# Performance work log

Hardware: AMD Instinct MI355X
Metric: run time of the kernel (lower is better)

Reference implementation:

```python
import jax, jax.numpy as jnp
import numpy as np

N_WIDTH = 16
N_ORDER = 3
N_ELEMENTS = 64
N_NODES = N_ELEMENTS * N_ORDER + 1  # 193
N_SAMPLES = 4096
X_MIN = 0.0
X_MAX = 1.0
NDIM_IN = 2


def setup_inputs() -> dict:
    key = jax.random.key(0)
    k1, k2 = jax.random.split(key)
    x = jax.random.uniform(k1, (N_SAMPLES, NDIM_IN), dtype=jnp.float32)  # in [x_min, x_max]
    # torch init is zeros; use small random values so outputs/grads are informative
    weight = 0.1 * jax.random.normal(k2, (N_WIDTH, N_NODES, NDIM_IN), dtype=jnp.float32)
    return {"x": x, "weight": weight}


def _lagrange_all(xr, nodes):
    """phi, dphi, ddphi of the (n_order+1) Lagrange basis at xr (S,W,D).
    Returns three arrays of shape (S,W,P,D), P = n_order+1. Loops are over the
    tiny fixed basis size only; everything is vectorized over (S,W,D)."""
    P = len(nodes)
    phi, dphi, ddphi = [], [], []
    for j in range(P):
        # value
        p = jnp.ones_like(xr)
        for m in range(P):
            if m != j:
                p = p * (xr - nodes[m]) / (nodes[j] - nodes[m])
        phi.append(p)
        # first derivative
        y1 = jnp.zeros_like(xr)
        for i in range(P):
            if i == j:
                continue
            k = jnp.full_like(xr, 1.0 / (nodes[j] - nodes[i]))
            for m in range(P):
                if m != i and m != j:
                    k = k * (xr - nodes[m]) / (nodes[j] - nodes[m])
            y1 = y1 + k
        dphi.append(y1)
        # second derivative
        y2 = jnp.zeros_like(xr)
        for i in range(P):
            if i == j:
                continue
            ks = jnp.zeros_like(xr)
            for m in range(P):
                if m != i and m != j:
                    kp = jnp.full_like(xr, 1.0 / (nodes[j] - nodes[m]))
                    for n in range(P):
                        if n != i and n != j and n != m:
                            kp = kp * (xr - nodes[n]) / (nodes[j] - nodes[n])
                    ks = ks + kp
            y2 = y2 + ks / (nodes[j] - nodes[i])
        ddphi.append(y2)
    return jnp.stack(phi, 2), jnp.stack(dphi, 2), jnp.stack(ddphi, 2)


def _forward(x, weight):
    S, W, D, P = N_SAMPLES, N_WIDTH, NDIM_IN, N_ORDER + 1
    xw = jnp.broadcast_to(x[:, None, :], (S, W, D))  # (S,W,D)
    x_shift = (N_NODES - 1) * (xw - X_MIN) / (X_MAX - X_MIN)
    id_el = jnp.clip(jnp.floor(x_shift / N_ORDER), 0, N_ELEMENTS - 1)
    nodes_l = (id_el * N_ORDER).astype(jnp.int32)  # (S,W,D), left node index
    # nodes_r - nodes_l == n_order
    x_ref = 2.0 * (x_shift - nodes_l) / N_ORDER - 1.0
    delta_x = 0.5 * N_ORDER * (X_MAX - X_MIN) / (N_NODES - 1)

    nodes = [float(v) for v in np.linspace(-1.0, 1.0, P)]
    phi_l, dphi_l, ddphi_l = _lagrange_all(x_ref, nodes)  # (S,W,P,D)
    dphi_l = dphi_l / delta_x
    ddphi_l = ddphi_l / (delta_x * delta_x)

    # Scatter local basis values into global node axis (vectorized replacement
    # of the quadruple Python loop in the original).
    ii = jnp.arange(S)[:, None, None, None]
    kk = jnp.arange(W)[None, :, None, None]
    dd = jnp.arange(D)[None, None, None, :]
    pp = nodes_l[:, :, None, :] + jnp.arange(P)[None, None, :, None]  # (S,W,P,D)
    zeros = jnp.zeros((S, W, N_NODES, D), dtype=x.dtype)
    phi = zeros.at[ii, kk, pp, dd].set(phi_l)
    dphi = zeros.at[ii, kk, pp, dd].set(dphi_l)
    ddphi = zeros.at[ii, kk, pp, dd].set(ddphi_l)

    t_ik = jnp.einsum('kpj,ikpj->ik', weight, phi)
    dt_ik = jnp.einsum('kpj,ikpj->ik', weight, dphi)
    ddt_ik = jnp.einsum('kpj,ikpj->ik', weight, ddphi)
    return t_ik, dt_ik, ddt_ik, phi, dphi, ddphi, delta_x


def reference(x, weight):
    # returns (t_ik, dt_ik, ddt_ik, phi_ikpj, dphi_ikpj, ddphi_ikpj, delta_x)
    return _forward(x, weight)
```

## Files before the change

kernel.cpp:

```cpp
#include <hip/hip_runtime.h>

constexpr int S  = 4096;
constexpr int W  = 16;
constexpr int NN = 193;
constexpr int DD = 2;
constexpr int SW = S * W;
constexpr int PHI_OFF = 3 * SW;
constexpr int PHI_SZ  = SW * NN * DD;
constexpr int DX_OFF  = PHI_OFF + 3 * PHI_SZ;

constexpr int ROW_F  = NN * DD;
constexpr int ROW_F2 = NN;
constexpr int CHUNK_F2 = W * ROW_F2;

__global__ __launch_bounds__(256)
void kan_fused_kernel(const float* __restrict__ x,
                      const float* __restrict__ w,
                      float* __restrict__ out) {
    const int i   = blockIdx.x;
    const int tid = threadIdx.x;

    __shared__ __align__(16) float row[3][ROW_F];
    __shared__ float vals[3][DD][4];
    __shared__ int   nls[DD];

    for (int idx = tid; idx < 3 * ROW_F; idx += 256)
        (&row[0][0])[idx] = 0.0f;

    if (tid < DD) {
        const int d = tid;
        float xv = x[i * DD + d];
        float xs = 192.0f * xv;
        float fe = floorf(xs / 3.0f);
        fe = fminf(fmaxf(fe, 0.0f), 63.0f);
        int nl = (int)(fe * 3.0f);
        nls[d] = nl;
        float xr = 2.0f * (xs - (float)nl) / 3.0f - 1.0f;

        float xp1 = xr + 1.0f;
        float xm1 = xr - 1.0f;
        float x2  = xr * xr;
        float x2m = x2 - (1.0f / 9.0f);
        const float c0 = 0.5625f;
        const float c1 = 1.6875f;

        vals[0][d][0] = -c0 * x2m * xm1;
        vals[0][d][1] =  c1 * xp1 * (xr - (1.0f / 3.0f)) * xm1;
        vals[0][d][2] = -c1 * xp1 * (xr + (1.0f / 3.0f)) * xm1;
        vals[0][d][3] =  c0 * xp1 * x2m;

        const float idx1 = 128.0f;
        vals[1][d][0] = -c0 * (3.0f * x2 - 2.0f * xr - (1.0f / 9.0f)) * idx1;
        vals[1][d][1] =  c1 * (3.0f * x2 - (2.0f / 3.0f) * xr - 1.0f) * idx1;
        vals[1][d][2] = -c1 * (3.0f * x2 + (2.0f / 3.0f) * xr - 1.0f) * idx1;
        vals[1][d][3] =  c0 * (3.0f * x2 + 2.0f * xr - (1.0f / 9.0f)) * idx1;

        const float idx2 = 16384.0f;
        vals[2][d][0] = -c0 * (6.0f * xr - 2.0f) * idx2;
        vals[2][d][1] =  c1 * (6.0f * xr - (2.0f / 3.0f)) * idx2;
        vals[2][d][2] = -c1 * (6.0f * xr + (2.0f / 3.0f)) * idx2;
        vals[2][d][3] =  c0 * (6.0f * xr + 2.0f) * idx2;
    }

    __syncthreads();

    if (tid < 24) {
        int a = tid >> 3;
        int r = tid & 7;
        int d = r >> 2;
        int p = r & 3;
        row[a][(nls[d] + p) * DD + d] = vals[a][d][p];
    }

    if (tid < 48) {
        int k = tid / 3;
        int a = tid % 3;
        float s = 0.0f;
#pragma unroll
        for (int d = 0; d < DD; ++d) {
            int base = k * (NN * DD) + nls[d] * DD + d;
#pragma unroll
            for (int p = 0; p < 4; ++p)
                s += w[base + p * DD] * vals[a][d][p];
        }
        out[a * SW + i * W + k] = s;
    }

    if (i == 0 && tid == 0)
        out[DX_OFF] = 0.0078125f;

    __syncthreads();

#pragma unroll
    for (int a = 0; a < 3; ++a) {
        float2* dst = (float2*)(out + PHI_OFF + a * PHI_SZ) + (size_t)i * CHUNK_F2;
        const float2* src = (const float2*)(&row[a][0]);
        for (int idx = tid; idx < CHUNK_F2; idx += 256) {
            int j = idx % ROW_F2;
            dst[idx] = src[j];
        }
    }
}

extern "C" void kernel_launch(void* const* d_in, const int* in_sizes, int n_in,
                              void* d_out, int out_size, void* d_ws, size_t ws_size,
                              hipStream_t stream) {
    const float* x = (const float*)d_in[0];
    const float* w = (const float*)d_in[1];
    float* out = (float*)d_out;

    kan_fused_kernel<<<S, 256, 0, stream>>>(x, w, out);
}
```

Baseline: 300.4 us.

## Split basis orders across blocks and generate phi rows in registers

Launches one block per (sample, derivative order) pair instead of one per sample. Each thread recomputes its basis values and builds the sparse phi rows directly in registers with select logic, so the shared-memory staging, zeroing and syncthreads go away. The rows are written with 16-byte vector stores instead of 8-byte ones. In exchange every thread redundantly evaluates the basis polynomials and does per-element compare/select work, and the grid is three times larger.

```diff
diff --git a/kernel.cpp b/kernel.cpp
--- a/kernel.cpp
+++ b/kernel.cpp
@@ -1,4 +1,6 @@
 #include <hip/hip_runtime.h>
+
+typedef float f32x4 __attribute__((ext_vector_type(4)));
 
 constexpr int S  = 4096;
 constexpr int W  = 16;
@@ -7,98 +9,109 @@
 constexpr int SW = S * W;
 constexpr int PHI_OFF = 3 * SW;
 constexpr int PHI_SZ  = SW * NN * DD;
-constexpr int DX_OFF  = PHI_OFF + 3 * PHI_SZ;
+constexpr long DX_OFF = (long)PHI_OFF + 3L * PHI_SZ;
 
-constexpr int ROW_F  = NN * DD;
-constexpr int ROW_F2 = NN;
-constexpr int CHUNK_F2 = W * ROW_F2;
+constexpr int ROW_F    = NN * DD;
+constexpr int CHUNK_F4 = W * ROW_F / 4;
+
+__device__ __forceinline__ void basis(int a, float xvd, int& nl,
+                                      float& c0, float& c1, float& c2, float& c3) {
+    float xs = 192.0f * xvd;
+    float fe = floorf(xs * (1.0f / 3.0f));
+    fe = fminf(fmaxf(fe, 0.0f), 63.0f);
+    nl = (int)(fe * 3.0f);
+    float xr = 2.0f * (xs - (float)nl) * (1.0f / 3.0f) - 1.0f;
+
+    const float k0 = 0.5625f;
+    const float k1 = 1.6875f;
+    float xp1 = xr + 1.0f;
+    float xm1 = xr - 1.0f;
+    float x2  = xr * xr;
+    float x2m = x2 - (1.0f / 9.0f);
+
+    if (a == 0) {
+        c0 = -k0 * x2m * xm1;
+        c1 =  k1 * xp1 * (xr - (1.0f / 3.0f)) * xm1;
+        c2 = -k1 * xp1 * (xr + (1.0f / 3.0f)) * xm1;
+        c3 =  k0 * xp1 * x2m;
+    } else if (a == 1) {
+        const float s1 = 128.0f;
+        c0 = -k0 * (3.0f * x2 - 2.0f * xr - (1.0f / 9.0f)) * s1;
+        c1 =  k1 * (3.0f * x2 - (2.0f / 3.0f) * xr - 1.0f) * s1;
+        c2 = -k1 * (3.0f * x2 + (2.0f / 3.0f) * xr - 1.0f) * s1;
+        c3 =  k0 * (3.0f * x2 + 2.0f * xr - (1.0f / 9.0f)) * s1;
+    } else {
+        const float s2 = 16384.0f;
+        c0 = -k0 * (6.0f * xr - 2.0f) * s2;
+        c1 =  k1 * (6.0f * xr - (2.0f / 3.0f)) * s2;
+        c2 = -k1 * (6.0f * xr + (2.0f / 3.0f)) * s2;
+        c3 =  k0 * (6.0f * xr + 2.0f) * s2;
+    }
+}
+
+__device__ __forceinline__ float pick4(int rel, float c0, float c1, float c2, float c3) {
+    float r = 0.0f;
+    r = (rel == 0) ? c0 : r;
+    r = (rel == 1) ? c1 : r;
+    r = (rel == 2) ? c2 : r;
+    r = (rel == 3) ? c3 : r;
+    return r;
+}
 
 __global__ __launch_bounds__(256)
-void kan_fused_kernel(const float* __restrict__ x,
-                      const float* __restrict__ w,
-                      float* __restrict__ out) {
-    const int i   = blockIdx.x;
+void kan_kernel(const float* __restrict__ x,
+                const float* __restrict__ w,
+                float* __restrict__ out) {
+    const int b   = blockIdx.x;
+    const int a   = b >> 12;
+    const int i   = b & 4095;
     const int tid = threadIdx.x;
 
-    __shared__ __align__(16) float row[3][ROW_F];
-    __shared__ float vals[3][DD][4];
-    __shared__ int   nls[DD];
+    const float xv0 = x[2 * i];
+    const float xv1 = x[2 * i + 1];
 
-    for (int idx = tid; idx < 3 * ROW_F; idx += 256)
-        (&row[0][0])[idx] = 0.0f;
+    int nl0, nl1;
+    float v00, v01, v02, v03, v10, v11, v12, v13;
+    basis(a, xv0, nl0, v00, v01, v02, v03);
+    basis(a, xv1, nl1, v10, v11, v12, v13);
 
-    if (tid < DD) {
-        const int d = tid;
-        float xv = x[i * DD + d];
-        float xs = 192.0f * xv;
-        float fe = floorf(xs / 3.0f);
-        fe = fminf(fmaxf(fe, 0.0f), 63.0f);
-        int nl = (int)(fe * 3.0f);
-        nls[d] = nl;
-        float xr = 2.0f * (xs - (float)nl) / 3.0f - 1.0f;
-
-        float xp1 = xr + 1.0f;
-        float xm1 = xr - 1.0f;
-        float x2  = xr * xr;
-        float x2m = x2 - (1.0f / 9.0f);
-        const float c0 = 0.5625f;
-        const float c1 = 1.6875f;
-
-        vals[0][d][0] = -c0 * x2m * xm1;
-        vals[0][d][1] =  c1 * xp1 * (xr - (1.0f / 3.0f)) * xm1;
-        vals[0][d][2] = -c1 * xp1 * (xr + (1.0f / 3.0f)) * xm1;
-        vals[0][d][3] =  c0 * xp1 * x2m;
-
-        const float idx1 = 128.0f;
-        vals[1][d][0] = -c0 * (3.0f * x2 - 2.0f * xr - (1.0f / 9.0f)) * idx1;
-        vals[1][d][1] =  c1 * (3.0f * x2 - (2.0f / 3.0f) * xr - 1.0f) * idx1;
-        vals[1][d][2] = -c1 * (3.0f * x2 + (2.0f / 3.0f) * xr - 1.0f) * idx1;
-        vals[1][d][3] =  c0 * (3.0f * x2 + 2.0f * xr - (1.0f / 9.0f)) * idx1;
-
-        const float idx2 = 16384.0f;
-        vals[2][d][0] = -c0 * (6.0f * xr - 2.0f) * idx2;
-        vals[2][d][1] =  c1 * (6.0f * xr - (2.0f / 3.0f)) * idx2;
-        vals[2][d][2] = -c1 * (6.0f * xr + (2.0f / 3.0f)) * idx2;
-        vals[2][d][3] =  c0 * (6.0f * xr + 2.0f) * idx2;
+    if (tid < W) {
+        const float* wk = w + tid * ROW_F;
+        float s = 0.0f;
+        s += wk[(nl0 + 0) * 2 + 0] * v00;
+        s += wk[(nl0 + 1) * 2 + 0] * v01;
+        s += wk[(nl0 + 2) * 2 + 0] * v02;
+        s += wk[(nl0 + 3) * 2 + 0] * v03;
+        s += wk[(nl1 + 0) * 2 + 1] * v10;
+        s += wk[(nl1 + 1) * 2 + 1] * v11;
+        s += wk[(nl1 + 2) * 2 + 1] * v12;
+        s += wk[(nl1 + 3) * 2 + 1] * v13;
+        out[a * SW + i * W + tid] = s;
     }
-
-    __syncthreads();
-
-    if (tid < 24) {
-        int a = tid >> 3;
-        int r = tid & 7;
-        int d = r >> 2;
-        int p = r & 3;
-        row[a][(nls[d] + p) * DD + d] = vals[a][d][p];
-    }
-
-    if (tid < 48) {
-        int k = tid / 3;
-        int a = tid % 3;
-        float s = 0.0f;
-#pragma unroll
-        for (int d = 0; d < DD; ++d) {
-            int base = k * (NN * DD) + nls[d] * DD + d;
-#pragma unroll
-            for (int p = 0; p < 4; ++p)
-                s += w[base + p * DD] * vals[a][d][p];
-        }
-        out[a * SW + i * W + k] = s;
-    }
-
-    if (i == 0 && tid == 0)
+    if (b == 0 && tid == 0)
         out[DX_OFF] = 0.0078125f;
 
-    __syncthreads();
+    f32x4* dst = (f32x4*)(out + PHI_OFF + (size_t)a * PHI_SZ)
+                 + (size_t)i * CHUNK_F4;
 
+    int e = 4 * tid;
+    if (e >= 772) e -= 772;
+    else if (e >= 386) e -= 386;
+
+    for (int p = tid; p < CHUNK_F4; p += 256) {
+        f32x4 vv;
 #pragma unroll
-    for (int a = 0; a < 3; ++a) {
-        float2* dst = (float2*)(out + PHI_OFF + a * PHI_SZ) + (size_t)i * CHUNK_F2;
-        const float2* src = (const float2*)(&row[a][0]);
-        for (int idx = tid; idx < CHUNK_F2; idx += 256) {
-            int j = idx % ROW_F2;
-            dst[idx] = src[j];
+        for (int j = 0; j < 4; ++j) {
+            int ee = e + j;
+            if (ee >= ROW_F) ee -= ROW_F;
+            int n = ee >> 1;
+            float p0 = pick4(n - nl0, v00, v01, v02, v03);
+            float p1 = pick4(n - nl1, v10, v11, v12, v13);
+            vv[j] = (ee & 1) ? p1 : p0;
         }
+        dst[p] = vv;
+        e += (256 * 4) % ROW_F;
+        if (e >= ROW_F) e -= ROW_F;
     }
 }
 
@@ -109,5 +122,5 @@
     const float* w = (const float*)d_in[1];
     float* out = (float*)d_out;
 
-    kan_fused_kernel<<<S, 256, 0, stream>>>(x, w, out);
+    kan_kernel<<<3 * S, 256, 0, stream>>>(x, w, out);
 }
```

After: 303.1 us. No clear change (+0.9%).
